# Kernel optimization log

Hardware: AMD Instinct MI355X
Metric: run time of the kernel (lower is better)

## Reference

```python
import jax, jax.numpy as jnp
import numpy as np

M = 5            # Anderson history size
LAM = 1e-4       # Tikhonov regularization on the Gram matrix
MAX_ITER = 50
TOL = 1e-5
BETA = 1.0
ALPHA = 0.9      # damping


def anderson(f, x0, m=M, lam=LAM, max_iter=MAX_ITER, tol=TOL, beta=BETA):
    """Anderson acceleration for fixed-point iteration (faithful to torch ref).

    x0: [bsz, L]. Variable history size n=min(k,m) is handled by masking the
    (m+1)x(m+1) system: inactive slots get an identity row -> alpha_j = 0.
    """
    bsz, L = x0.shape
    dt = x0.dtype
    F0 = f(x0)
    F1 = f(F0)
    X = jnp.zeros((bsz, m, L), dt).at[:, 0].set(x0).at[:, 1].set(F0)
    Fh = jnp.zeros((bsz, m, L), dt).at[:, 0].set(F0).at[:, 1].set(F1)
    eye_m = jnp.eye(m, dtype=dt)

    def body(carry):
        k, X, Fh, _ = carry
        n = jnp.minimum(k, m)
        active = (jnp.arange(m) < n).astype(dt)          # [m]
        G = Fh - X                                        # inactive rows are zero
        Hc = jnp.einsum('bil,bjl->bij', G, G) + lam * eye_m
        m2 = active[:, None] * active[None, :]
        # zero out inactive rows/cols, put 1 on their diagonal (=> alpha_j = 0)
        Hc = Hc * m2 + eye_m * (1.0 - active)
        H = jnp.zeros((bsz, m + 1, m + 1), dt)
        H = H.at[:, 0, 1:].set(active).at[:, 1:, 0].set(active).at[:, 1:, 1:].set(Hc)
        y = jnp.zeros((bsz, m + 1, 1), dt).at[:, 0, 0].set(1.0)
        alpha_c = jnp.linalg.solve(H, y)[:, 1:, 0]        # [bsz, m]
        xnew = beta * jnp.einsum('bm,bml->bl', alpha_c, Fh) \
             + (1.0 - beta) * jnp.einsum('bm,bml->bl', alpha_c, X)
        slot = k % m
        X = X.at[:, slot].set(xnew)
        fnew = f(xnew)
        Fh = Fh.at[:, slot].set(fnew)
        res = jnp.linalg.norm(fnew - xnew) / (1e-5 + jnp.linalg.norm(fnew))
        return (k + 1, X, Fh, res)

    def cond(carry):
        k, _, _, res = carry
        return jnp.logical_and(k < max_iter, res >= tol)

    k, X, Fh, res = jax.lax.while_loop(
        cond, body, (jnp.array(2), X, Fh, jnp.array(np.inf, dt)))
    return X[:, (k - 1) % m]


def make_f(x, maskf, W, b, alpha):
    """Damped forward step: z -> softmax_ch((1-a)z + a*Conv(mask-inject(z)))."""
    bsz, C, H, Wd = x.shape

    def f(zflat):
        z = zflat.reshape(bsz, C, H, Wd)
        zm = z * (1.0 - maskf) + maskf * x               # inject observed parts
        lin = jax.lax.conv_general_dilated(
            zm, W, window_strides=(1, 1), padding='SAME',
            dimension_numbers=('NCHW', 'OIHW', 'NCHW')) + b[None, :, None, None]
        pre = (1.0 - alpha) * z + alpha * lin
        return jax.nn.softmax(pre, axis=1).reshape(bsz, -1)

    return f


def setup_inputs() -> dict:
    key = jax.random.key(0)
    k1, k2, k3 = jax.random.split(key, 3)
    bsz, C, H, Wd = 32, 128, 32, 32
    x = jax.random.normal(k1, (bsz, C, H, Wd), jnp.float32)
    mask = jax.random.randint(k2, (bsz, 1, H, Wd), 0, 2).astype(jnp.int32)
    W = jax.random.normal(k3, (C, C, 3, 3), jnp.float32) * 0.05  # keep map contractive
    b = jnp.zeros((C,), jnp.float32)
    return {"x": x, "W": W, "b": b, "mask": mask}


def reference(x, W, b, mask):
    bsz, C, H, Wd = x.shape
    maskf = mask.astype(x.dtype)
    f = make_f(x, maskf, W, b, ALPHA)
    # z_start = softmax(zeros) over channel dim -> uniform 1/C
    z0 = jnp.full((bsz, C * H * Wd), 1.0 / C, x.dtype)
    zstar = anderson(f, z0)
    zn = f(zstar)            # one extra step, as in the torch forward
    return zn                # [bsz, C*H*W]
```

## Files before the change

### kernel.cpp

```cpp
#include <hip/hip_runtime.h>


typedef unsigned short u16;
using short8 = __attribute__((ext_vector_type(8))) short;
using f32x4  = __attribute__((ext_vector_type(4))) float;

#define SLOT 4194304

struct Ctrl { int done; int last_slot; };

__device__ __forceinline__ u16 f2bf(float f) {
  unsigned u = __builtin_bit_cast(unsigned, f);
  unsigned r = (u + 0x7FFFu + ((u >> 16) & 1u)) >> 16;
  return (u16)r;
}
__device__ __forceinline__ float bf2f(u16 h) {
  unsigned u = ((unsigned)h) << 16;
  return __builtin_bit_cast(float, u);
}

__global__ void __launch_bounds__(256) k_prepw(const float* __restrict__ W,
    u16* __restrict__ Wb, Ctrl* ctrl) {
  if (blockIdx.x == 0 && threadIdx.x == 0) { ctrl->done = 0; ctrl->last_slot = 4; }
  int t = blockIdx.x * 256 + threadIdx.x;
  int o = t >> 14;
  int rem = t & 16383;
  int cout = rem >> 7, cin = rem & 127;
  float v = W[(size_t)cout * 1152 + (size_t)cin * 9 + o];
  Wb[(size_t)o * 16384 + (size_t)cout * 128 + cin] = f2bf(v);
}

__global__ void __launch_bounds__(256) k_prepx(const float* __restrict__ x,
    u16* __restrict__ xsw) {
  int t = blockIdx.x * 256 + threadIdx.x;
  int g = t >> 15, p = t & 32767;
  int nb = p >> 10, gp = p & 1023, px = p & 31;
  short8 xv;
#pragma unroll
  for (int u = 0; u < 8; ++u) {
    float v = x[(size_t)nb * 131072 + (size_t)(g * 8 + u) * 1024 + gp];
    xv[u] = (short)f2bf(v);
  }
  *(short8*)(xsw + (size_t)p * 128 + (size_t)((g ^ (px & 7)) << 3)) = xv;
}

__global__ void __launch_bounds__(512)
__attribute__((amdgpu_waves_per_eu(2, 4)))
k_iter(
    const int e,
    const u16* __restrict__ xsw, const int* __restrict__ mask_,
    const u16* __restrict__ Wb, const float* __restrict__ bias,
    float* __restrict__ Fhp, u16* __restrict__ FhH, u16* __restrict__ Gp,
    float* __restrict__ gram, float* __restrict__ gpart,
    float* __restrict__ resp, Ctrl* __restrict__ ctrl)
{
  __shared__ char smem[39552];
  char*  As       = smem;
  float* rowmax_s = (float*)(smem + 34816);
  float* rowsum_s = (float*)(smem + 36864);
  float* red      = (float*)(smem + 38912);
  float* alpha_s  = (float*)(smem + 39168);
  float* res_s    = (float*)(smem + 39188);
  int*   mk_s     = (int*)(smem + 39296);

  if (ctrl->done) return;

  const int tid = threadIdx.x;
  const int wc = tid >> 6, lane = tid & 63;
  const int lhi = lane >> 4, llo = lane & 15;
  const int bhw = blockIdx.x;
  const int lbid = ((bhw & 7) << 6) + (bhw >> 3);
  const int n = lbid >> 4, y0 = (lbid & 15) << 1;
  const int gpix0 = (n << 10) + (y0 << 5);
  const int colc = (wc << 4) + llo;
  const int slot = e % 5;
  const int nact = e < 5 ? e : 5;
  const size_t base = ((size_t)lbid * 512 + tid) * 16;

  if (e >= 3) {
    if (tid < 64) {
      float sd = 0.f, sf = 0.f;
      for (int i = tid; i < 512; i += 64) { sd += resp[2 * i]; sf += resp[2 * i + 1]; }
#pragma unroll
      for (int off = 1; off < 64; off <<= 1) { sd += __shfl_xor(sd, off); sf += __shfl_xor(sf, off); }
      if (tid == 0) res_s[0] = sqrtf(sd) / (1e-5f + sqrtf(sf));
    }
    __syncthreads();
    if (res_s[0] < 1e-5f) {
      if (tid == 0) { ctrl->done = 1; ctrl->last_slot = (e - 1) % 5; }
      return;
    }
  }

  if (tid < 64) mk_s[tid] = mask_[gpix0 + tid];
  if (e >= 1 && tid >= 64 && tid < 69) {
    int j = tid - 64;
    float s = 0.f;
#pragma unroll
    for (int c = 0; c < 16; ++c) s += gpart[(size_t)((n << 4) + c) * 5 + j];
    int sp = (e - 1) % 5;
    gram[n * 25 + sp * 5 + j] = s;
    gram[n * 25 + j * 5 + sp] = s;
  }
  __syncthreads();
  if (e >= 2) {
    if (tid == 0) {
      float A[6][7];
      for (int i = 0; i < 5; ++i)
        for (int j = 0; j < 5; ++j)
          A[i + 1][j + 1] = (i < nact && j < nact)
              ? gram[n * 25 + i * 5 + j] + ((i == j) ? 1e-4f : 0.f)
              : ((i == j) ? 1.f : 0.f);
      A[0][0] = 0.f;
      for (int j = 0; j < 5; ++j) { float aj = (j < nact) ? 1.f : 0.f; A[0][j + 1] = aj; A[j + 1][0] = aj; }
      A[0][6] = 1.f;
      for (int i = 1; i < 6; ++i) A[i][6] = 0.f;
      for (int c = 0; c < 6; ++c) {
        int p = c; float mx = fabsf(A[c][c]);
        for (int r = c + 1; r < 6; ++r) { float v = fabsf(A[r][c]); if (v > mx) { mx = v; p = r; } }
        if (p != c) for (int q = c; q < 7; ++q) { float tmp = A[c][q]; A[c][q] = A[p][q]; A[p][q] = tmp; }
        float piv = A[c][c];
        for (int r = c + 1; r < 6; ++r) {
          float fr = A[r][c] / piv;
          for (int q = c; q < 7; ++q) A[r][q] -= fr * A[c][q];
        }
      }
      float sol[6];
      for (int r = 5; r >= 0; --r) {
        float s = A[r][6];
        for (int q = r + 1; q < 6; ++q) s -= A[r][q] * sol[q];
        sol[r] = s / A[r][r];
      }
      for (int j = 0; j < 5; ++j) alpha_s[j] = sol[j + 1];
    }
  } else if (tid < 5) {
    alpha_s[tid] = (tid == 0) ? 1.f : 0.f;
  }
  __syncthreads();

  float a0 = 1.f, a1 = 0.f, a2 = 0.f, a3 = 0.f, a4 = 0.f;
  if (e >= 1) { a0 = alpha_s[0]; a1 = alpha_s[1]; a2 = alpha_s[2]; a3 = alpha_s[3]; a4 = alpha_s[4]; }

  f32x4 zv[4];
  if (e == 0) {
    const f32x4 cz = {0.0078125f, 0.0078125f, 0.0078125f, 0.0078125f};
    zv[0] = cz; zv[1] = cz; zv[2] = cz; zv[3] = cz;
  } else {
    const float* fb = Fhp + base;
#pragma unroll
    for (int q = 0; q < 4; ++q) zv[q] = a0 * *(const f32x4*)(fb + q * 4);
    if (nact > 1) {
#pragma unroll
      for (int q = 0; q < 4; ++q) zv[q] += a1 * *(const f32x4*)(fb + SLOT + q * 4);
    }
    if (nact > 2) {
#pragma unroll
      for (int q = 0; q < 4; ++q) zv[q] += a2 * *(const f32x4*)(fb + 2 * SLOT + q * 4);
    }
    if (nact > 3) {
#pragma unroll
      for (int q = 0; q < 4; ++q) zv[q] += a3 * *(const f32x4*)(fb + 3 * SLOT + q * 4);
    }
    if (nact > 4) {
#pragma unroll
      for (int q = 0; q < 4; ++q) zv[q] += a4 * *(const f32x4*)(fb + 4 * SLOT + q * 4);
    }
  }

#pragma unroll
  for (int m2 = 0; m2 < 4; ++m2)
#pragma unroll
    for (int rr = 0; rr < 4; ++rr) {
      int p = (m2 << 4) + (lhi << 2) + rr;
      int px = p & 31, row = 1 + (p >> 5);
      int sg = (colc >> 3) ^ (px & 7);
      u16 w;
      if (mk_s[p])
        w = xsw[(size_t)(gpix0 + p) * 128 + (sg << 3) + (colc & 7)];
      else
        w = f2bf(zv[m2][rr]);
      *(u16*)(As + row * 8704 + ((px + 1) << 8) + (sg << 4) + ((colc & 7) << 1)) = w;
    }

#pragma unroll
  for (int uu = 0; uu < 2; ++uu) {
    int u = (uu << 9) + tid;
    int row = (u >> 9) * 3;
    int gy = y0 - 1 + row;
    int idx = u & 511;
    int px = idx >> 4, grp = idx & 15;
    char* dst = As + row * 8704 + ((px + 1) << 8) + ((grp ^ (px & 7)) << 4);
    short8 w = {0, 0, 0, 0, 0, 0, 0, 0};
    if ((unsigned)gy < 32u) {
      int gpix = (n << 10) + (gy << 5) + px;
      size_t off = (size_t)gpix * 128 + (size_t)((grp ^ (px & 7)) << 3);
      if (mask_[gpix]) {
        w = *(const short8*)(xsw + off);
      } else if (e == 0) {
#pragma unroll
        for (int i = 0; i < 8; ++i) w[i] = (short)0x3C00;
      } else {
        f32x4 va, vb;
        short8 h = *(const short8*)(FhH + off);
#pragma unroll
        for (int i = 0; i < 4; ++i) { va[i] = a0 * bf2f((u16)h[i]); vb[i] = a0 * bf2f((u16)h[4 + i]); }
        if (nact > 1) {
          h = *(const short8*)(FhH + SLOT + off);
#pragma unroll
          for (int i = 0; i < 4; ++i) { va[i] += a1 * bf2f((u16)h[i]); vb[i] += a1 * bf2f((u16)h[4 + i]); }
        }
        if (nact > 2) {
          h = *(const short8*)(FhH + 2 * (size_t)SLOT + off);
#pragma unroll
          for (int i = 0; i < 4; ++i) { va[i] += a2 * bf2f((u16)h[i]); vb[i] += a2 * bf2f((u16)h[4 + i]); }
        }
        if (nact > 3) {
          h = *(const short8*)(FhH + 3 * (size_t)SLOT + off);
#pragma unroll
          for (int i = 0; i < 4; ++i) { va[i] += a3 * bf2f((u16)h[i]); vb[i] += a3 * bf2f((u16)h[4 + i]); }
        }
        if (nact > 4) {
          h = *(const short8*)(FhH + 4 * (size_t)SLOT + off);
#pragma unroll
          for (int i = 0; i < 4; ++i) { va[i] += a4 * bf2f((u16)h[i]); vb[i] += a4 * bf2f((u16)h[4 + i]); }
        }
#pragma unroll
        for (int i = 0; i < 4; ++i) { w[i] = (short)f2bf(va[i]); w[4 + i] = (short)f2bf(vb[i]); }
      }
    }
    *(short8*)dst = w;
  }
  if (tid < 128) {
    int r = tid >> 5, cc = tid & 31;
    int col = (cc < 16) ? 0 : 33, gc = cc & 15;
    f32x4 zz = {0.f, 0.f, 0.f, 0.f};
    *(f32x4*)(As + r * 8704 + (col << 8) + (gc << 4)) = zz;
  }
  __syncthreads();

  f32x4 acc[4];
  {
    const f32x4 z4 = {0.f, 0.f, 0.f, 0.f};
    acc[0] = z4; acc[1] = z4; acc[2] = z4; acc[3] = z4;
  }
#pragma unroll
  for (int o = 0; o < 9; ++o) {
    const int dy = o / 3, dx = o % 3;
    short8 bfr[4];
#pragma unroll
    for (int kk = 0; kk < 4; ++kk)
      bfr[kk] = *(const short8*)(Wb + o * 16384 + colc * 128 + ((kk << 2) + lhi) * 8);
#pragma unroll
    for (int kk = 0; kk < 4; ++kk) {
      const int kg = (kk << 2) + lhi;
#pragma unroll
      for (int m2 = 0; m2 < 4; ++m2) {
        int p = (m2 << 4) + llo;
        int r = (p >> 5) + dy, cl = (p & 31) + dx;
        int sg = kg ^ ((cl - 1) & 7);
        short8 af = *(const short8*)(As + r * 8704 + (cl << 8) + (sg << 4));
        acc[m2] = __builtin_amdgcn_mfma_f32_16x16x32_bf16(af, bfr[kk], acc[m2], 0, 0, 0);
      }
    }
  }

  const float bc = bias[colc];
#pragma unroll
  for (int m2 = 0; m2 < 4; ++m2)
#pragma unroll
    for (int rr = 0; rr < 4; ++rr)
      acc[m2][rr] = 0.1f * zv[m2][rr] + 0.9f * (acc[m2][rr] + bc);
#pragma unroll
  for (int m2 = 0; m2 < 4; ++m2)
#pragma unroll
    for (int rr = 0; rr < 4; ++rr) {
      float v = acc[m2][rr];
      v = fmaxf(v, __shfl_xor(v, 1)); v = fmaxf(v, __shfl_xor(v, 2));
      v = fmaxf(v, __shfl_xor(v, 4)); v = fmaxf(v, __shfl_xor(v, 8));
      if (llo == 0) rowmax_s[((m2 << 4) + (lhi << 2) + rr) * 8 + wc] = v;
    }
  __syncthreads();
#pragma unroll
  for (int m2 = 0; m2 < 4; ++m2)
#pragma unroll
    for (int rr = 0; rr < 4; ++rr) {
      int p = (m2 << 4) + (lhi << 2) + rr;
      f32x4 m0 = *(const f32x4*)&rowmax_s[p * 8];
      f32x4 m1 = *(const f32x4*)&rowmax_s[p * 8 + 4];
      float M = fmaxf(fmaxf(fmaxf(m0[0], m0[1]), fmaxf(m0[2], m0[3])),
                      fmaxf(fmaxf(m1[0], m1[1]), fmaxf(m1[2], m1[3])));
      float ev = __expf(acc[m2][rr] - M);
      acc[m2][rr] = ev;
      float s = ev;
      s += __shfl_xor(s, 1); s += __shfl_xor(s, 2);
      s += __shfl_xor(s, 4); s += __shfl_xor(s, 8);
      if (llo == 0) rowsum_s[p * 8 + wc] = s;
    }
  __syncthreads();

  float sd = 0.f, sf = 0.f;
  float gd16[16];
#pragma unroll
  for (int m2 = 0; m2 < 4; ++m2) {
    f32x4 fr;
#pragma unroll
    for (int rr = 0; rr < 4; ++rr) {
      int p = (m2 << 4) + (lhi << 2) + rr;
      f32x4 s0 = *(const f32x4*)&rowsum_s[p * 8];
      f32x4 s1 = *(const f32x4*)&rowsum_s[p * 8 + 4];
      float S = s0[0] + s0[1] + s0[2] + s0[3] + s1[0] + s1[1] + s1[2] + s1[3];
      float fnew = acc[m2][rr] * (1.0f / S);
      fr[rr] = fnew;
      float gd = fnew - zv[m2][rr];
      gd16[m2 * 4 + rr] = gd;
      sd += gd * gd; sf += fnew * fnew;
      int px = p & 31;
      FhH[(size_t)slot * SLOT + (size_t)(gpix0 + p) * 128 +
          ((((colc >> 3) ^ (px & 7)) << 3) | (colc & 7))] = f2bf(fnew);
    }
    *(f32x4*)(Fhp + (size_t)slot * SLOT + base + m2 * 4) = fr;
  }
  {
    short8 h0, h1;
#pragma unroll
    for (int i = 0; i < 8; ++i) { h0[i] = (short)f2bf(gd16[i]); h1[i] = (short)f2bf(gd16[8 + i]); }
    u16* Gs = Gp + (size_t)slot * SLOT + base;
    *(short8*)(Gs) = h0;
    *(short8*)(Gs + 8) = h1;
    const int jmax = e < 4 ? e : 4;
    float gacc[5];
#pragma unroll
    for (int j = 0; j < 5; ++j) {
      if (j > jmax) { gacc[j] = 0.f; continue; }
      if (j == slot) {
        float a = 0.f;
#pragma unroll
        for (int i = 0; i < 16; ++i) a += gd16[i] * gd16[i];
        gacc[j] = a;
      } else {
        short8 q0 = *(const short8*)(Gp + (size_t)j * SLOT + base);
        short8 q1 = *(const short8*)(Gp + (size_t)j * SLOT + base + 8);
        float a = 0.f;
#pragma unroll
        for (int i = 0; i < 8; ++i)
          a += gd16[i] * bf2f((u16)q0[i]) + gd16[8 + i] * bf2f((u16)q1[i]);
        gacc[j] = a;
      }
    }
    float vals[7] = {gacc[0], gacc[1], gacc[2], gacc[3], gacc[4], sd, sf};
#pragma unroll
    for (int i = 0; i < 7; ++i) {
      float v = vals[i];
#pragma unroll
      for (int off = 1; off < 64; off <<= 1) v += __shfl_xor(v, off);
      if (lane == 0) red[wc * 8 + i] = v;
    }
  }
  __syncthreads();
  if (tid < 7) {
    float s = 0.f;
#pragma unroll
    for (int w = 0; w < 8; ++w) s += red[w * 8 + tid];
    if (tid < 5)       gpart[(size_t)lbid * 5 + tid] = s;
    else if (tid == 5) resp[lbid * 2] = s;
    else               resp[lbid * 2 + 1] = s;
  }
}

__global__ void __launch_bounds__(512) k_out(const float* __restrict__ Fhp,
    const Ctrl* __restrict__ ctrl, float* __restrict__ out)
{
  __shared__ float T[64 * 129];
  int slot = ctrl->last_slot;
  const int tid = threadIdx.x;
  const int wc = tid >> 6, lane = tid & 63;
  const int lhi = lane >> 4, llo = lane & 15;
  const int bhw = blockIdx.x;
  const int lbid = ((bhw & 7) << 6) + (bhw >> 3);
  const int n = lbid >> 4, y0 = (lbid & 15) << 1;
  const size_t base = (size_t)slot * SLOT + ((size_t)lbid * 512 + tid) * 16;
#pragma unroll
  for (int m2 = 0; m2 < 4; ++m2) {
    f32x4 v = *(const f32x4*)(Fhp + base + m2 * 4);
#pragma unroll
    for (int rr = 0; rr < 4; ++rr) {
      int p = (m2 << 4) + (lhi << 2) + rr;
      T[p * 129 + (wc << 4) + llo] = v[rr];
    }
  }
  __syncthreads();
  int c = tid >> 2, q = tid & 3;
  int row = q >> 1, xs = (q & 1) << 4;
  float* ob = out + (((size_t)(n << 7) + c) << 10) + ((y0 + row) << 5) + xs;
#pragma unroll
  for (int i2 = 0; i2 < 4; ++i2) {
    f32x4 v;
#pragma unroll
    for (int i = 0; i < 4; ++i) v[i] = T[((row << 5) + xs + (i2 << 2) + i) * 129 + c];
    *(f32x4*)(ob + (i2 << 2)) = v;
  }
}

extern "C" void kernel_launch(void* const* d_in, const int* in_sizes, int n_in,
                              void* d_out, int out_size, void* d_ws, size_t ws_size,
                              hipStream_t stream) {
  const float* x    = (const float*)d_in[0];
  const float* W    = (const float*)d_in[1];
  const float* bias = (const float*)d_in[2];
  const int*   mask = (const int*)d_in[3];
  float* out = (float*)d_out;
  char* ws = (char*)d_ws;

  float* Fhp   = (float*)(ws + 0);
  u16*   FhH   = (u16*)(ws + 83886080);
  u16*   Gp    = (u16*)(ws + 125829120);
  u16*   xsw   = (u16*)(ws + 167772160);
  u16*   Wb    = (u16*)(ws + 176160768);
  float* gram  = (float*)(ws + 176455680);
  float* gpart = (float*)(ws + 176458880);
  float* resp  = (float*)(ws + 176469120);
  Ctrl*  ctrl  = (Ctrl*)(ws + 176473216);

  k_prepw<<<576, 256, 0, stream>>>(W, Wb, ctrl);
  k_prepx<<<2048, 256, 0, stream>>>(x, xsw);
  for (int e = 0; e < 50; ++e)
    k_iter<<<512, 512, 0, stream>>>(e, xsw, mask, Wb, bias,
                                    Fhp, FhH, Gp, gram, gpart, resp, ctrl);
  k_out<<<512, 512, 0, stream>>>(Fhp, ctrl, out);
  (void)in_sizes; (void)n_in; (void)out_size; (void)ws_size;
}
```

Before: 468.7 us.

## Retile iteration kernel to one image row per 256-thread block

The fused Anderson iteration kernel now handles one output row (32 pixels) per block with 4 waves, each covering 32 output channels through two MFMA column fragments, instead of two rows per 512-thread block with 16 channels per wave. The grid doubles to 1024 blocks, shared memory drops to a 3-row halo, and mask values for the halo are staged in LDS rather than reloaded from global memory. The goal is higher occupancy and reuse of each A fragment across two MFMAs. In exchange, the halo is proportionally larger (3 rows loaded per output row), which means more redundant halo loads and Anderson mixing work. The softmax cross-wave reductions, Gram partials and output transpose kernel are adjusted to match.

```diff
diff --git a/kernel.cpp b/kernel.cpp
--- a/kernel.cpp
+++ b/kernel.cpp
@@ -44,8 +44,8 @@
   *(short8*)(xsw + (size_t)p * 128 + (size_t)((g ^ (px & 7)) << 3)) = xv;
 }
 
-__global__ void __launch_bounds__(512)
-__attribute__((amdgpu_waves_per_eu(2, 4)))
+__global__ void __launch_bounds__(256)
+__attribute__((amdgpu_waves_per_eu(5)))
 k_iter(
     const int e,
     const u16* __restrict__ xsw, const int* __restrict__ mask_,
@@ -54,33 +54,32 @@
     float* __restrict__ gram, float* __restrict__ gpart,
     float* __restrict__ resp, Ctrl* __restrict__ ctrl)
 {
-  __shared__ char smem[39552];
+  __shared__ char smem[27776];
   char*  As       = smem;
-  float* rowmax_s = (float*)(smem + 34816);
-  float* rowsum_s = (float*)(smem + 36864);
-  float* red      = (float*)(smem + 38912);
-  float* alpha_s  = (float*)(smem + 39168);
-  float* res_s    = (float*)(smem + 39188);
-  int*   mk_s     = (int*)(smem + 39296);
+  float* rowmax_s = (float*)(smem + 26112);
+  float* rowsum_s = (float*)(smem + 26624);
+  float* red      = (float*)(smem + 27136);
+  float* alpha_s  = (float*)(smem + 27264);
+  float* res_s    = (float*)(smem + 27284);
+  int*   mk3      = (int*)(smem + 27392);
 
   if (ctrl->done) return;
 
   const int tid = threadIdx.x;
-  const int wc = tid >> 6, lane = tid & 63;
+  const int wv = tid >> 6, lane = tid & 63;
   const int lhi = lane >> 4, llo = lane & 15;
   const int bhw = blockIdx.x;
-  const int lbid = ((bhw & 7) << 6) + (bhw >> 3);
-  const int n = lbid >> 4, y0 = (lbid & 15) << 1;
+  const int lbid = ((bhw & 7) << 7) + (bhw >> 3);
+  const int n = lbid >> 5, y0 = lbid & 31;
   const int gpix0 = (n << 10) + (y0 << 5);
-  const int colc = (wc << 4) + llo;
   const int slot = e % 5;
   const int nact = e < 5 ? e : 5;
-  const size_t base = ((size_t)lbid * 512 + tid) * 16;
+  const size_t base = ((size_t)lbid * 256 + tid) * 16;
 
   if (e >= 3) {
     if (tid < 64) {
       float sd = 0.f, sf = 0.f;
-      for (int i = tid; i < 512; i += 64) { sd += resp[2 * i]; sf += resp[2 * i + 1]; }
+      for (int i = tid; i < 1024; i += 64) { sd += resp[2 * i]; sf += resp[2 * i + 1]; }
 #pragma unroll
       for (int off = 1; off < 64; off <<= 1) { sd += __shfl_xor(sd, off); sf += __shfl_xor(sf, off); }
       if (tid == 0) res_s[0] = sqrtf(sd) / (1e-5f + sqrtf(sf));
@@ -92,12 +91,16 @@
     }
   }
 
-  if (tid < 64) mk_s[tid] = mask_[gpix0 + tid];
-  if (e >= 1 && tid >= 64 && tid < 69) {
-    int j = tid - 64;
+  if (tid < 96) {
+    int r = tid >> 5, xx = tid & 31;
+    int gy = y0 - 1 + r;
+    mk3[tid] = ((unsigned)gy < 32u) ? mask_[(n << 10) + (gy << 5) + xx] : 0;
+  }
+  if (e >= 1 && tid >= 96 && tid < 101) {
+    int j = tid - 96;
     float s = 0.f;
 #pragma unroll
-    for (int c = 0; c < 16; ++c) s += gpart[(size_t)((n << 4) + c) * 5 + j];
+    for (int c = 0; c < 32; ++c) s += gpart[(size_t)((n << 5) + c) * 5 + j];
     int sp = (e - 1) % 5;
     gram[n * 25 + sp * 5 + j] = s;
     gram[n * 25 + j * 5 + sp] = s;
@@ -168,33 +171,35 @@
   }
 
 #pragma unroll
-  for (int m2 = 0; m2 < 4; ++m2)
-#pragma unroll
-    for (int rr = 0; rr < 4; ++rr) {
-      int p = (m2 << 4) + (lhi << 2) + rr;
-      int px = p & 31, row = 1 + (p >> 5);
-      int sg = (colc >> 3) ^ (px & 7);
-      u16 w;
-      if (mk_s[p])
-        w = xsw[(size_t)(gpix0 + p) * 128 + (sg << 3) + (colc & 7)];
-      else
-        w = f2bf(zv[m2][rr]);
-      *(u16*)(As + row * 8704 + ((px + 1) << 8) + (sg << 4) + ((colc & 7) << 1)) = w;
-    }
-
-#pragma unroll
-  for (int uu = 0; uu < 2; ++uu) {
-    int u = (uu << 9) + tid;
-    int row = (u >> 9) * 3;
-    int gy = y0 - 1 + row;
+  for (int m2 = 0; m2 < 2; ++m2)
+#pragma unroll
+    for (int nf = 0; nf < 2; ++nf)
+#pragma unroll
+      for (int rr = 0; rr < 4; ++rr) {
+        int p = (m2 << 4) + (lhi << 2) + rr;
+        int ch = (wv << 5) + (nf << 4) + llo;
+        int sg = (ch >> 3) ^ (p & 7);
+        u16 w;
+        if (mk3[32 + p])
+          w = xsw[(size_t)(gpix0 + p) * 128 + (sg << 3) + (ch & 7)];
+        else
+          w = f2bf(zv[(m2 << 1) + nf][rr]);
+        *(u16*)(As + 8704 + ((p + 1) << 8) + (sg << 4) + ((ch & 7) << 1)) = w;
+      }
+
+#pragma unroll 2
+  for (int uu = 0; uu < 4; ++uu) {
+    int u = (uu << 8) + tid;
+    int row3 = u >> 9;
+    int gy = y0 - 1 + (row3 << 1);
     int idx = u & 511;
     int px = idx >> 4, grp = idx & 15;
-    char* dst = As + row * 8704 + ((px + 1) << 8) + ((grp ^ (px & 7)) << 4);
+    char* dst = As + (row3 << 1) * 8704 + ((px + 1) << 8) + ((grp ^ (px & 7)) << 4);
     short8 w = {0, 0, 0, 0, 0, 0, 0, 0};
     if ((unsigned)gy < 32u) {
       int gpix = (n << 10) + (gy << 5) + px;
       size_t off = (size_t)gpix * 128 + (size_t)((grp ^ (px & 7)) << 3);
-      if (mask_[gpix]) {
+      if (mk3[(row3 << 6) + px]) {
         w = *(const short8*)(xsw + off);
       } else if (e == 0) {
 #pragma unroll
@@ -230,7 +235,7 @@
     }
     *(short8*)dst = w;
   }
-  if (tid < 128) {
+  if (tid < 96) {
     int r = tid >> 5, cc = tid & 31;
     int col = (cc < 16) ? 0 : 33, gc = cc & 15;
     f32x4 zz = {0.f, 0.f, 0.f, 0.f};
@@ -238,92 +243,111 @@
   }
   __syncthreads();
 
-  f32x4 acc[4];
+  f32x4 acc[2][2];
   {
     const f32x4 z4 = {0.f, 0.f, 0.f, 0.f};
-    acc[0] = z4; acc[1] = z4; acc[2] = z4; acc[3] = z4;
+    acc[0][0] = z4; acc[0][1] = z4; acc[1][0] = z4; acc[1][1] = z4;
   }
 #pragma unroll
   for (int o = 0; o < 9; ++o) {
     const int dy = o / 3, dx = o % 3;
-    short8 bfr[4];
-#pragma unroll
-    for (int kk = 0; kk < 4; ++kk)
-      bfr[kk] = *(const short8*)(Wb + o * 16384 + colc * 128 + ((kk << 2) + lhi) * 8);
+    short8 bfr[2][4];
+#pragma unroll
+    for (int nf = 0; nf < 2; ++nf)
+#pragma unroll
+      for (int kk = 0; kk < 4; ++kk) {
+        int ch = (wv << 5) + (nf << 4) + llo;
+        bfr[nf][kk] = *(const short8*)(Wb + o * 16384 + ch * 128 + ((kk << 2) + lhi) * 8);
+      }
 #pragma unroll
     for (int kk = 0; kk < 4; ++kk) {
       const int kg = (kk << 2) + lhi;
 #pragma unroll
-      for (int m2 = 0; m2 < 4; ++m2) {
+      for (int m2 = 0; m2 < 2; ++m2) {
         int p = (m2 << 4) + llo;
-        int r = (p >> 5) + dy, cl = (p & 31) + dx;
+        int cl = p + dx;
         int sg = kg ^ ((cl - 1) & 7);
-        short8 af = *(const short8*)(As + r * 8704 + (cl << 8) + (sg << 4));
-        acc[m2] = __builtin_amdgcn_mfma_f32_16x16x32_bf16(af, bfr[kk], acc[m2], 0, 0, 0);
-      }
-    }
-  }
-
-  const float bc = bias[colc];
-#pragma unroll
-  for (int m2 = 0; m2 < 4; ++m2)
-#pragma unroll
-    for (int rr = 0; rr < 4; ++rr)
-      acc[m2][rr] = 0.1f * zv[m2][rr] + 0.9f * (acc[m2][rr] + bc);
-#pragma unroll
-  for (int m2 = 0; m2 < 4; ++m2)
+        short8 af = *(const short8*)(As + dy * 8704 + (cl << 8) + (sg << 4));
+#pragma unroll
+        for (int nf = 0; nf < 2; ++nf)
+          acc[m2][nf] = __builtin_amdgcn_mfma_f32_16x16x32_bf16(af, bfr[nf][kk], acc[m2][nf], 0, 0, 0);
+      }
+    }
+  }
+
+  const float bc0 = bias[(wv << 5) + llo];
+  const float bc1 = bias[(wv << 5) + 16 + llo];
+#pragma unroll
+  for (int m2 = 0; m2 < 2; ++m2)
 #pragma unroll
     for (int rr = 0; rr < 4; ++rr) {
-      float v = acc[m2][rr];
+      acc[m2][0][rr] = 0.1f * zv[m2 << 1][rr] + 0.9f * (acc[m2][0][rr] + bc0);
+      acc[m2][1][rr] = 0.1f * zv[(m2 << 1) + 1][rr] + 0.9f * (acc[m2][1][rr] + bc1);
+    }
+#pragma unroll
+  for (int m2 = 0; m2 < 2; ++m2)
+#pragma unroll
+    for (int rr = 0; rr < 4; ++rr) {
+      float v = fmaxf(acc[m2][0][rr], acc[m2][1][rr]);
       v = fmaxf(v, __shfl_xor(v, 1)); v = fmaxf(v, __shfl_xor(v, 2));
       v = fmaxf(v, __shfl_xor(v, 4)); v = fmaxf(v, __shfl_xor(v, 8));
-      if (llo == 0) rowmax_s[((m2 << 4) + (lhi << 2) + rr) * 8 + wc] = v;
-    }
-  __syncthreads();
-#pragma unroll
-  for (int m2 = 0; m2 < 4; ++m2)
+      if (llo == 0) rowmax_s[(((m2 << 4) + (lhi << 2) + rr) << 2) + wv] = v;
+    }
+  __syncthreads();
+#pragma unroll
+  for (int m2 = 0; m2 < 2; ++m2)
 #pragma unroll
     for (int rr = 0; rr < 4; ++rr) {
       int p = (m2 << 4) + (lhi << 2) + rr;
-      f32x4 m0 = *(const f32x4*)&rowmax_s[p * 8];
-      f32x4 m1 = *(const f32x4*)&rowmax_s[p * 8 + 4];
-      float M = fmaxf(fmaxf(fmaxf(m0[0], m0[1]), fmaxf(m0[2], m0[3])),
-                      fmaxf(fmaxf(m1[0], m1[1]), fmaxf(m1[2], m1[3])));
-      float ev = __expf(acc[m2][rr] - M);
-      acc[m2][rr] = ev;
-      float s = ev;
+      f32x4 m0 = *(const f32x4*)&rowmax_s[p << 2];
+      float M = fmaxf(fmaxf(m0[0], m0[1]), fmaxf(m0[2], m0[3]));
+      float e0 = __expf(acc[m2][0][rr] - M);
+      float e1 = __expf(acc[m2][1][rr] - M);
+      acc[m2][0][rr] = e0; acc[m2][1][rr] = e1;
+      float s = e0 + e1;
       s += __shfl_xor(s, 1); s += __shfl_xor(s, 2);
       s += __shfl_xor(s, 4); s += __shfl_xor(s, 8);
-      if (llo == 0) rowsum_s[p * 8 + wc] = s;
+      if (llo == 0) rowsum_s[(p << 2) + wv] = s;
     }
   __syncthreads();
 
   float sd = 0.f, sf = 0.f;
-  float gd16[16];
-#pragma unroll
-  for (int m2 = 0; m2 < 4; ++m2) {
-    f32x4 fr;
+#pragma unroll
+  for (int m2 = 0; m2 < 2; ++m2) {
+    f32x4 fr0, fr1;
 #pragma unroll
     for (int rr = 0; rr < 4; ++rr) {
       int p = (m2 << 4) + (lhi << 2) + rr;
-      f32x4 s0 = *(const f32x4*)&rowsum_s[p * 8];
-      f32x4 s1 = *(const f32x4*)&rowsum_s[p * 8 + 4];
-      float S = s0[0] + s0[1] + s0[2] + s0[3] + s1[0] + s1[1] + s1[2] + s1[3];
-      float fnew = acc[m2][rr] * (1.0f / S);
-      fr[rr] = fnew;
-      float gd = fnew - zv[m2][rr];
-      gd16[m2 * 4 + rr] = gd;
-      sd += gd * gd; sf += fnew * fnew;
-      int px = p & 31;
-      FhH[(size_t)slot * SLOT + (size_t)(gpix0 + p) * 128 +
-          ((((colc >> 3) ^ (px & 7)) << 3) | (colc & 7))] = f2bf(fnew);
-    }
-    *(f32x4*)(Fhp + (size_t)slot * SLOT + base + m2 * 4) = fr;
+      f32x4 s0 = *(const f32x4*)&rowsum_s[p << 2];
+      float S = s0[0] + s0[1] + s0[2] + s0[3];
+      float invS = 1.0f / S;
+      float f0 = acc[m2][0][rr] * invS;
+      float f1 = acc[m2][1][rr] * invS;
+      acc[m2][0][rr] = f0; acc[m2][1][rr] = f1;
+      fr0[rr] = f0; fr1[rr] = f1;
+      float g0 = f0 - zv[m2 << 1][rr];
+      float g1 = f1 - zv[(m2 << 1) + 1][rr];
+      sd += g0 * g0 + g1 * g1; sf += f0 * f0 + f1 * f1;
+      int ch0 = (wv << 5) + llo, ch1 = ch0 + 16;
+      size_t rb = (size_t)slot * SLOT + (size_t)(gpix0 + p) * 128;
+      FhH[rb + ((((ch0 >> 3) ^ (p & 7)) << 3) | (ch0 & 7))] = f2bf(f0);
+      FhH[rb + ((((ch1 >> 3) ^ (p & 7)) << 3) | (ch1 & 7))] = f2bf(f1);
+    }
+    *(f32x4*)(Fhp + (size_t)slot * SLOT + base + (m2 << 3)) = fr0;
+    *(f32x4*)(Fhp + (size_t)slot * SLOT + base + (m2 << 3) + 4) = fr1;
   }
   {
     short8 h0, h1;
 #pragma unroll
-    for (int i = 0; i < 8; ++i) { h0[i] = (short)f2bf(gd16[i]); h1[i] = (short)f2bf(gd16[8 + i]); }
+    for (int m2 = 0; m2 < 2; ++m2)
+#pragma unroll
+      for (int nf = 0; nf < 2; ++nf)
+#pragma unroll
+        for (int rr = 0; rr < 4; ++rr) {
+          int q = (((m2 << 1) + nf) << 2) + rr;
+          u16 gb16 = f2bf(acc[m2][nf][rr] - zv[(m2 << 1) + nf][rr]);
+          if (q < 8) h0[q] = (short)gb16; else h1[q - 8] = (short)gb16;
+        }
     u16* Gs = Gp + (size_t)slot * SLOT + base;
     *(short8*)(Gs) = h0;
     *(short8*)(Gs + 8) = h1;
@@ -335,15 +359,30 @@
       if (j == slot) {
         float a = 0.f;
 #pragma unroll
-        for (int i = 0; i < 16; ++i) a += gd16[i] * gd16[i];
+        for (int m2 = 0; m2 < 2; ++m2)
+#pragma unroll
+          for (int nf = 0; nf < 2; ++nf)
+#pragma unroll
+            for (int rr = 0; rr < 4; ++rr) {
+              float gd = acc[m2][nf][rr] - zv[(m2 << 1) + nf][rr];
+              a += gd * gd;
+            }
         gacc[j] = a;
       } else {
         short8 q0 = *(const short8*)(Gp + (size_t)j * SLOT + base);
         short8 q1 = *(const short8*)(Gp + (size_t)j * SLOT + base + 8);
         float a = 0.f;
 #pragma unroll
-        for (int i = 0; i < 8; ++i)
-          a += gd16[i] * bf2f((u16)q0[i]) + gd16[8 + i] * bf2f((u16)q1[i]);
+        for (int m2 = 0; m2 < 2; ++m2)
+#pragma unroll
+          for (int nf = 0; nf < 2; ++nf)
+#pragma unroll
+            for (int rr = 0; rr < 4; ++rr) {
+              int q = (((m2 << 1) + nf) << 2) + rr;
+              float gd = acc[m2][nf][rr] - zv[(m2 << 1) + nf][rr];
+              float hv = bf2f((u16)(q < 8 ? q0[q] : q1[q - 8]));
+              a += gd * hv;
+            }
         gacc[j] = a;
       }
     }
@@ -353,50 +392,51 @@
       float v = vals[i];
 #pragma unroll
       for (int off = 1; off < 64; off <<= 1) v += __shfl_xor(v, off);
-      if (lane == 0) red[wc * 8 + i] = v;
+      if (lane == 0) red[(wv << 3) + i] = v;
     }
   }
   __syncthreads();
   if (tid < 7) {
     float s = 0.f;
 #pragma unroll
-    for (int w = 0; w < 8; ++w) s += red[w * 8 + tid];
+    for (int w = 0; w < 4; ++w) s += red[(w << 3) + tid];
     if (tid < 5)       gpart[(size_t)lbid * 5 + tid] = s;
     else if (tid == 5) resp[lbid * 2] = s;
     else               resp[lbid * 2 + 1] = s;
   }
 }
 
-__global__ void __launch_bounds__(512) k_out(const float* __restrict__ Fhp,
+__global__ void __launch_bounds__(256) k_out(const float* __restrict__ Fhp,
     const Ctrl* __restrict__ ctrl, float* __restrict__ out)
 {
-  __shared__ float T[64 * 129];
+  __shared__ float T[32 * 132];
   int slot = ctrl->last_slot;
   const int tid = threadIdx.x;
-  const int wc = tid >> 6, lane = tid & 63;
+  const int wv = tid >> 6, lane = tid & 63;
   const int lhi = lane >> 4, llo = lane & 15;
-  const int bhw = blockIdx.x;
-  const int lbid = ((bhw & 7) << 6) + (bhw >> 3);
-  const int n = lbid >> 4, y0 = (lbid & 15) << 1;
-  const size_t base = (size_t)slot * SLOT + ((size_t)lbid * 512 + tid) * 16;
-#pragma unroll
-  for (int m2 = 0; m2 < 4; ++m2) {
-    f32x4 v = *(const f32x4*)(Fhp + base + m2 * 4);
-#pragma unroll
-    for (int rr = 0; rr < 4; ++rr) {
-      int p = (m2 << 4) + (lhi << 2) + rr;
-      T[p * 129 + (wc << 4) + llo] = v[rr];
-    }
-  }
-  __syncthreads();
-  int c = tid >> 2, q = tid & 3;
-  int row = q >> 1, xs = (q & 1) << 4;
-  float* ob = out + (((size_t)(n << 7) + c) << 10) + ((y0 + row) << 5) + xs;
+  const int lbid = blockIdx.x;
+  const int n = lbid >> 5, y0 = lbid & 31;
+  const size_t base = (size_t)slot * SLOT + ((size_t)lbid * 256 + tid) * 16;
+#pragma unroll
+  for (int m2 = 0; m2 < 2; ++m2)
+#pragma unroll
+    for (int nf = 0; nf < 2; ++nf) {
+      f32x4 v = *(const f32x4*)(Fhp + base + (((m2 << 1) + nf) << 2));
+#pragma unroll
+      for (int rr = 0; rr < 4; ++rr) {
+        int p = (m2 << 4) + (lhi << 2) + rr;
+        int ch = (wv << 5) + (nf << 4) + llo;
+        T[p * 132 + ch] = v[rr];
+      }
+    }
+  __syncthreads();
+  int c = tid >> 1, h = tid & 1;
+  float* ob = out + (((size_t)(n << 7) + c) << 10) + (y0 << 5) + (h << 4);
 #pragma unroll
   for (int i2 = 0; i2 < 4; ++i2) {
     f32x4 v;
 #pragma unroll
-    for (int i = 0; i < 4; ++i) v[i] = T[((row << 5) + xs + (i2 << 2) + i) * 129 + c];
+    for (int i = 0; i < 4; ++i) v[i] = T[((h << 4) + (i2 << 2) + i) * 132 + c];
     *(f32x4*)(ob + (i2 << 2)) = v;
   }
 }
@@ -418,14 +458,14 @@
   u16*   Wb    = (u16*)(ws + 176160768);
   float* gram  = (float*)(ws + 176455680);
   float* gpart = (float*)(ws + 176458880);
-  float* resp  = (float*)(ws + 176469120);
-  Ctrl*  ctrl  = (Ctrl*)(ws + 176473216);
+  float* resp  = (float*)(ws + 176479360);
+  Ctrl*  ctrl  = (Ctrl*)(ws + 176487552);
 
   k_prepw<<<576, 256, 0, stream>>>(W, Wb, ctrl);
   k_prepx<<<2048, 256, 0, stream>>>(x, xsw);
   for (int e = 0; e < 50; ++e)
-    k_iter<<<512, 512, 0, stream>>>(e, xsw, mask, Wb, bias,
-                                    Fhp, FhH, Gp, gram, gpart, resp, ctrl);
-  k_out<<<512, 512, 0, stream>>>(Fhp, ctrl, out);
+    k_iter<<<1024, 256, 0, stream>>>(e, xsw, mask, Wb, bias,
+                                     Fhp, FhH, Gp, gram, gpart, resp, ctrl);
+  k_out<<<1024, 256, 0, stream>>>(Fhp, ctrl, out);
   (void)in_sizes; (void)n_in; (void)out_size; (void)ws_size;
 }
```

Measured after the change: 479.5 us. 1.02x slower.
